# Kernel tuning notes

Measured on AMD Instinct MI355X. Metric: run time of the kernel, lower is better.

Reference implementation:

```python
import jax, jax.numpy as jnp
import numpy as np

EPS = 1e-8
NEG = -float(2 ** 31)

B, N, D = 8, 2048, 256  # batch, nodes, input_dim == output_dim


def setup_inputs() -> dict:
    key = jax.random.key(0)
    ks = jax.random.split(key, 8)
    x = jax.random.normal(ks[0], (B, N, D), dtype=jnp.float32)
    x_topic = jax.random.normal(ks[1], (B, N, D), dtype=jnp.float32)
    adj_mask = jax.random.randint(ks[2], (B, N, N), 0, 2, dtype=jnp.int32)
    s = 1.0 / np.sqrt(D)
    W = jax.random.uniform(ks[3], (D, D), minval=-s, maxval=s, dtype=jnp.float32)
    # GRUCell params (torch layout: [3*H, in] with gate order r, z, n)
    W_ih = jax.random.uniform(ks[4], (3 * D, D), minval=-s, maxval=s, dtype=jnp.float32)
    W_hh = jax.random.uniform(ks[5], (3 * D, D), minval=-s, maxval=s, dtype=jnp.float32)
    b_ih = jax.random.uniform(ks[6], (3 * D,), minval=-s, maxval=s, dtype=jnp.float32)
    b_hh = jax.random.uniform(ks[7], (3 * D,), minval=-s, maxval=s, dtype=jnp.float32)
    return {"adj_mask": adj_mask, "x": x, "x_topic": x_topic,
            "W": W, "W_ih": W_ih, "W_hh": W_hh, "b_ih": b_ih, "b_hh": b_hh}


def _gru_cell(inp, h, W_ih, W_hh, b_ih, b_hh):
    # torch.nn.GRUCell math, gate order (r, z, n)
    gi = inp @ W_ih.T + b_ih
    gh = h @ W_hh.T + b_hh
    i_r, i_z, i_n = jnp.split(gi, 3, axis=-1)
    h_r, h_z, h_n = jnp.split(gh, 3, axis=-1)
    r = jax.nn.sigmoid(i_r + h_r)
    z = jax.nn.sigmoid(i_z + h_z)
    n = jnp.tanh(i_n + r * h_n)
    return (1.0 - z) * n + z * h


def reference(adj_mask, x, x_topic, W, W_ih, W_hh, b_ih, b_hh):
    # Wh: [B, N, H]
    Wh = jnp.einsum('bnd,dh->bnh', x, W)
    # pairwise cosine similarity via normalized gram matrix (no N x N x D intermediate)
    nrm = jnp.linalg.norm(x_topic, axis=-1)            # [B, N]
    dots = jnp.einsum('bnd,bmd->bnm', x_topic, x_topic)
    e = dots / jnp.maximum(nrm[:, :, None] * nrm[:, None, :], EPS)
    scores = jnp.where(adj_mask > 0, e, NEG)
    attention = jax.nn.softmax(scores, axis=-1)        # [B, N, N]
    graph_out = jnp.einsum('bnm,bmh->bnh', attention, Wh)
    out = _gru_cell(graph_out, x, W_ih, W_hh, b_ih, b_hh)
    return out
```

## Files before the change

kernel.cpp:

```cpp
#include <hip/hip_runtime.h>
#include <hip/hip_bf16.h>

#define B_ 8
#define N_ 2048
#define D_ 256

using bf16 = __hip_bfloat16;
typedef short v8s __attribute__((ext_vector_type(8)));
typedef float v4f __attribute__((ext_vector_type(4)));
typedef float v16f __attribute__((ext_vector_type(16)));
typedef unsigned int u32;

__device__ __forceinline__ v4f mfma16(v8s a, v8s b, v4f c) {
  return __builtin_amdgcn_mfma_f32_16x16x32_bf16(a, b, c, 0, 0, 0);
}
__device__ __forceinline__ v16f mfma32(v8s a, v8s b, v16f c) {
  return __builtin_amdgcn_mfma_f32_32x32x16_bf16(a, b, c, 0, 0, 0);
}
__device__ __forceinline__ v8s ldb8(const bf16* p) {
  return *reinterpret_cast<const v8s*>(p);
}
__device__ __forceinline__ void glds16(const void* g, void* l) {
  __builtin_amdgcn_global_load_lds((const __attribute__((address_space(1))) u32*)g,
                                   (__attribute__((address_space(3))) u32*)l, 16, 0, 0);
}
__device__ __forceinline__ unsigned short f2bu(float f) {
  bf16 b = __float2bfloat16(f);
  return *reinterpret_cast<unsigned short*>(&b);
}
__device__ __forceinline__ float bs2f(short s) {
  union { u32 i; float f; } v; v.i = ((u32)(unsigned short)s) << 16; return v.f;
}
__device__ __forceinline__ float lo16(u32 u) { union {u32 i; float f;} v; v.i = u << 16; return v.f; }
__device__ __forceinline__ float hi16(u32 u) { union {u32 i; float f;} v; v.i = u & 0xffff0000u; return v.f; }
__device__ __forceinline__ u32 pack2(float a, float b) {
  return (u32)f2bu(a) | ((u32)f2bu(b) << 16);
}
__device__ __forceinline__ float fsigmoid(float x) { return 1.0f / (1.0f + __expf(-x)); }
__device__ __forceinline__ float ftanh(float x) {
  float ax = fabsf(x);
  float t = __expf(-2.0f * ax);
  float r = (1.0f - t) / (1.0f + t);
  return copysignf(r, x);
}

__global__ __launch_bounds__(256) void k_cvt(const float* __restrict__ src,
                                             bf16* __restrict__ dst, int n4) {
  int i = blockIdx.x * 256 + threadIdx.x;
  if (i >= n4) return;
  float4 v = reinterpret_cast<const float4*>(src)[i];
  ushort4 o;
  o.x = f2bu(v.x); o.y = f2bu(v.y); o.z = f2bu(v.z); o.w = f2bu(v.w);
  reinterpret_cast<ushort4*>(dst)[i] = o;
}

__global__ __launch_bounds__(256) void k_cvtn(const float* __restrict__ xt,
                                              bf16* __restrict__ dst) {
  int i = blockIdx.x * 256 + threadIdx.x;
  float4 v = reinterpret_cast<const float4*>(xt)[i];
  float s = v.x * v.x + v.y * v.y + v.z * v.z + v.w * v.w;
#pragma unroll
  for (int off = 32; off > 0; off >>= 1) s += __shfl_xor(s, off);
  float rinv = 1.0f / fmaxf(sqrtf(s), 1e-8f);
  ushort4 o;
  o.x = f2bu(v.x * rinv); o.y = f2bu(v.y * rinv);
  o.z = f2bu(v.z * rinv); o.w = f2bu(v.w * rinv);
  reinterpret_cast<ushort4*>(dst)[i] = o;
}

__global__ __launch_bounds__(256) void k_prep(const float* __restrict__ W,
                                              bf16* __restrict__ Wt,
                                              const float* __restrict__ Wih,
                                              bf16* __restrict__ Wih16,
                                              const float* __restrict__ Whh,
                                              bf16* __restrict__ Whh16) {
  int blk = blockIdx.x;
  if (blk < 256) {
    int idx = blk * 256 + threadIdx.x;
    int d = idx >> 8, h = idx & 255;
    Wt[h * 256 + d] = __float2bfloat16(W[idx]);
  } else if (blk < 448) {
    int i = (blk - 256) * 256 + threadIdx.x;
    float4 v = reinterpret_cast<const float4*>(Wih)[i];
    ushort4 o;
    o.x = f2bu(v.x); o.y = f2bu(v.y); o.z = f2bu(v.z); o.w = f2bu(v.w);
    reinterpret_cast<ushort4*>(Wih16)[i] = o;
  } else {
    int i = (blk - 448) * 256 + threadIdx.x;
    float4 v = reinterpret_cast<const float4*>(Whh)[i];
    ushort4 o;
    o.x = f2bu(v.x); o.y = f2bu(v.y); o.z = f2bu(v.z); o.w = f2bu(v.w);
    reinterpret_cast<ushort4*>(Whh16)[i] = o;
  }
}

__global__ __launch_bounds__(256) void k_packT(const int* __restrict__ adj,
                                               u32* __restrict__ maskT) {
  int bi = blockIdx.x;
  int bg = bi >> 1, half = bi & 1;
  const int* base = adj + (size_t)bg * 32 * 2048;
  int c0 = half * 1024 + threadIdx.x * 4;
  u32 w0 = 0, w1 = 0, w2 = 0, w3 = 0;
#pragma unroll 4
  for (int r = 0; r < 32; r++) {
    int4 v = *reinterpret_cast<const int4*>(base + r * 2048 + c0);
    w0 |= (u32)(v.x > 0) << r;
    w1 |= (u32)(v.y > 0) << r;
    w2 |= (u32)(v.z > 0) << r;
    w3 |= (u32)(v.w > 0) << r;
  }
  uint4 o; o.x = w0; o.y = w1; o.z = w2; o.w = w3;
  *reinterpret_cast<uint4*>(maskT + (size_t)bg * 2048 + c0) = o;
}

__global__ __launch_bounds__(256) void k_wht(const bf16* __restrict__ x,
                                             const bf16* __restrict__ Wt,
                                             bf16* __restrict__ WhT) {
  int wid = blockIdx.x * 4 + (threadIdx.x >> 6);
  int lane = threadIdx.x & 63, lr = lane & 15, quad = lane >> 4;
  int b = wid >> 9;
  int rem = wid & 511;
  int h0 = (rem >> 5) << 4;
  int m0 = (rem & 31) << 6;

  v8s a[8];
  const bf16* arow = Wt + (size_t)(h0 + lr) * D_ + quad * 8;
#pragma unroll
  for (int ks = 0; ks < 8; ks++) a[ks] = ldb8(arow + ks * 32);

  const bf16* xb = x + (size_t)b * N_ * D_;
#pragma unroll
  for (int mt = 0; mt < 4; mt++) {
    v4f acc = {0.f, 0.f, 0.f, 0.f};
    const bf16* brow = xb + (size_t)(m0 + mt * 16 + lr) * D_ + quad * 8;
#pragma unroll
    for (int ks = 0; ks < 8; ks++) acc = mfma16(a[ks], ldb8(brow + ks * 32), acc);
    bf16* o = WhT + ((size_t)b * D_ + h0 + quad * 4) * N_ + m0 + mt * 16 + lr;
#pragma unroll
    for (int r = 0; r < 4; r++) o[(size_t)r * N_] = __float2bfloat16(acc[r]);
  }
}

__global__ __launch_bounds__(256, 2) void k_attn(const bf16* __restrict__ xtn,
                                                 const u32* __restrict__ maskT,
                                                 const bf16* __restrict__ WhT,
                                                 bf16* __restrict__ po,
                                                 float* __restrict__ pls) {
  __shared__ __align__(16) bf16 xts[2][32 * 256];
  __shared__ __align__(16) bf16 whs[2][256 * 32];
  __shared__ __align__(16) bf16 pbuf[4][32 * 40];

  const int tid = threadIdx.x;
  const int w = tid >> 6, lane = tid & 63;
  const int l5 = lane >> 5, l31 = lane & 31;
  const int b = blockIdx.x & 7;
  const int nt = (blockIdx.x >> 3) & 15;
  const int mh = blockIdx.x >> 7;
  const int n0w = nt * 128 + w * 32;
  const int mbase = mh * 512;

  const bf16* xtb = xtn + (size_t)b * N_ * D_;
  const bf16* whb = WhT + (size_t)b * D_ * N_;

  v8s q[16];
  {
    const bf16* qrow = xtb + (size_t)(n0w + l31) * D_ + l5 * 8;
#pragma unroll
    for (int kt = 0; kt < 16; kt++) q[kt] = ldb8(qrow + kt * 16);
  }
  const u32* mrow = maskT + ((size_t)(b * 64 + nt * 4 + w)) * 2048 + mbase + l31;

  auto stage = [&](int d, int m0) {
    const char* gx = (const char*)(xtb + (size_t)m0 * D_);
    char* lx = ((char*)xts[d]) + w * 4096;
#pragma unroll
    for (int j = 0; j < 4; j++) {
      int m = w * 8 + j * 2 + l5;
      int gg = l31 ^ (m & 7);
      glds16(gx + (size_t)m * 512 + gg * 16, lx + j * 1024);
    }
    char* lw = ((char*)whs[d]) + w * 4096;
#pragma unroll
    for (int j = 0; j < 4; j++) {
      int h = w * 64 + j * 16 + (lane >> 2);
      int g = (lane & 3) ^ ((lane >> 3) & 3);
      glds16((const char*)(whb + (size_t)h * N_ + m0) + g * 16, lw + j * 1024);
    }
  };

  v16f o[8];
#pragma unroll
  for (int t = 0; t < 8; t++) o[t] = (v16f)(0.f);
  float lsum = 0.f;

  u32 mword = mrow[0];
  stage(0, mbase);

#pragma unroll 1
  for (int ii = 0; ii < 16; ii++) {
    const int d = ii & 1;
    __syncthreads();
    if (ii + 1 < 16) stage(1 - d, mbase + (ii + 1) * 32);
    u32 mnext = (ii + 1 < 16) ? mrow[(ii + 1) * 32] : 0u;

    v16f s = (v16f)(0.f);
    const bf16* xb = xts[d] + l31 * 256;
#pragma unroll
    for (int kt = 0; kt < 16; kt++) {
      int g = ((kt * 2 + l5) ^ (l31 & 7)) * 8;
      s = mfma32(q[kt], ldb8(xb + g), s);
    }

    bf16* pb = pbuf[w];
#pragma unroll
    for (int j = 0; j < 16; j++) {
      int row = (j & 3) + 8 * (j >> 2) + 4 * l5;
      float p = ((mword >> row) & 1u) ? __expf(s[j]) : 0.f;
      pb[row * 40 + l31] = __float2bfloat16(p);
    }
    mword = mnext;

    v8s pa0 = ldb8(pb + l31 * 40 + l5 * 8);
    v8s pa1 = ldb8(pb + l31 * 40 + 16 + l5 * 8);
#pragma unroll
    for (int e = 0; e < 8; e++) lsum += bs2f(pa0[e]) + bs2f(pa1[e]);

#pragma unroll
    for (int ht = 0; ht < 8; ht++) {
      const bf16* wb = whs[d] + (ht * 32 + l31) * 32;
      int s0 = (l5 ^ ((l31 >> 1) & 3)) * 8;
      int s1 = ((2 + l5) ^ ((l31 >> 1) & 3)) * 8;
      o[ht] = mfma32(pa0, ldb8(wb + s0), o[ht]);
      o[ht] = mfma32(pa1, ldb8(wb + s1), o[ht]);
    }
  }

  lsum += __shfl_xor(lsum, 32);
  if (lane < 32) pls[(size_t)mh * (B_ * N_) + b * N_ + n0w + l31] = lsum;

  bf16* pob = po + (size_t)mh * ((size_t)B_ * N_ * D_) + ((size_t)b * N_ + n0w) * D_;
#pragma unroll
  for (int ht = 0; ht < 8; ht++) {
#pragma unroll
    for (int j = 0; j < 16; j++) {
      int row = (j & 3) + 8 * (j >> 2) + 4 * l5;
      pob[(size_t)row * D_ + ht * 32 + l31] = __float2bfloat16(o[ht][j]);
    }
  }
}

__global__ __launch_bounds__(256) void k_comb(const bf16* __restrict__ po,
                                              const float* __restrict__ pls,
                                              bf16* __restrict__ gout) {
  int idx = blockIdx.x * 256 + threadIdx.x;
  int row = idx >> 5;
  const int R = B_ * N_;
  float inv = 1.0f / (pls[row] + pls[R + row] + pls[2 * R + row] + pls[3 * R + row]);
  const size_t S = (size_t)B_ * N_ * D_ / 8;
  const uint4* p = (const uint4*)po;
  uint4 a = p[idx], c = p[idx + S], e = p[idx + 2 * S], f = p[idx + 3 * S];
  uint4 o;
  o.x = pack2((lo16(a.x)+lo16(c.x)+lo16(e.x)+lo16(f.x)) * inv,
              (hi16(a.x)+hi16(c.x)+hi16(e.x)+hi16(f.x)) * inv);
  o.y = pack2((lo16(a.y)+lo16(c.y)+lo16(e.y)+lo16(f.y)) * inv,
              (hi16(a.y)+hi16(c.y)+hi16(e.y)+hi16(f.y)) * inv);
  o.z = pack2((lo16(a.z)+lo16(c.z)+lo16(e.z)+lo16(f.z)) * inv,
              (hi16(a.z)+hi16(c.z)+hi16(e.z)+hi16(f.z)) * inv);
  o.w = pack2((lo16(a.w)+lo16(c.w)+lo16(e.w)+lo16(f.w)) * inv,
              (hi16(a.w)+hi16(c.w)+hi16(e.w)+hi16(f.w)) * inv);
  reinterpret_cast<uint4*>(gout)[idx] = o;
}

__global__ __launch_bounds__(256) void k_gru(const bf16* __restrict__ gout,
                                             const bf16* __restrict__ x16,
                                             const bf16* __restrict__ Wih,
                                             const bf16* __restrict__ Whh,
                                             const float* __restrict__ bih,
                                             const float* __restrict__ bhh,
                                             const float* __restrict__ x32,
                                             float* __restrict__ out) {
  int wid = blockIdx.x * 4 + (threadIdx.x >> 6);
  int lane = threadIdx.x & 63, lr = lane & 15, quad = lane >> 4;
  int rs = wid >> 4;
  int col0 = (wid & 15) << 4;
  int row0 = rs << 6;
  int col = col0 + lr;

  float bi[3], bh[3];
#pragma unroll
  for (int g = 0; g < 3; g++) {
    bi[g] = bih[g * 256 + col];
    bh[g] = bhh[g * 256 + col];
  }
  v4f aI[3][4], aH[3][4];
#pragma unroll
  for (int g = 0; g < 3; g++)
#pragma unroll
    for (int rt = 0; rt < 4; rt++) {
      aI[g][rt] = (v4f){0, 0, 0, 0};
      aH[g][rt] = (v4f){0, 0, 0, 0};
    }

#pragma unroll 2
  for (int ks = 0; ks < 8; ks++) {
    int k0 = ks * 32 + quad * 8;
    v8s wI[3], wH[3];
#pragma unroll
    for (int g = 0; g < 3; g++) {
      wI[g] = ldb8(Wih + (size_t)(g * 256 + col0 + lr) * 256 + k0);
      wH[g] = ldb8(Whh + (size_t)(g * 256 + col0 + lr) * 256 + k0);
    }
#pragma unroll
    for (int rt = 0; rt < 4; rt++) {
      v8s aG = ldb8(gout + (size_t)(row0 + rt * 16 + lr) * 256 + k0);
      v8s aX = ldb8(x16 + (size_t)(row0 + rt * 16 + lr) * 256 + k0);
#pragma unroll
      for (int g = 0; g < 3; g++) {
        aI[g][rt] = mfma16(aG, wI[g], aI[g][rt]);
        aH[g][rt] = mfma16(aX, wH[g], aH[g][rt]);
      }
    }
  }

#pragma unroll
  for (int rt = 0; rt < 4; rt++) {
    int rowb = row0 + rt * 16 + quad * 4;
#pragma unroll
    for (int r = 0; r < 4; r++) {
      float ir  = aI[0][rt][r] + bi[0];
      float iz  = aI[1][rt][r] + bi[1];
      float in_ = aI[2][rt][r] + bi[2];
      float hr  = aH[0][rt][r] + bh[0];
      float hz  = aH[1][rt][r] + bh[1];
      float hn  = aH[2][rt][r] + bh[2];
      float rg = fsigmoid(ir + hr);
      float zg = fsigmoid(iz + hz);
      float ng = ftanh(in_ + rg * hn);
      float hv = x32[(size_t)(rowb + r) * 256 + col];
      out[(size_t)(rowb + r) * 256 + col] = (1.0f - zg) * ng + zg * hv;
    }
  }
}

extern "C" void kernel_launch(void* const* d_in, const int* in_sizes, int n_in,
                              void* d_out, int out_size, void* d_ws, size_t ws_size,
                              hipStream_t stream) {
  const int*   adj = (const int*)d_in[0];
  const float* x   = (const float*)d_in[1];
  const float* xt  = (const float*)d_in[2];
  const float* W   = (const float*)d_in[3];
  const float* Wih = (const float*)d_in[4];
  const float* Whh = (const float*)d_in[5];
  const float* bih = (const float*)d_in[6];
  const float* bhh = (const float*)d_in[7];
  float* out = (float*)d_out;

  char* ws = (char*)d_ws;
  bf16*  xb16   = (bf16*)(ws);
  bf16*  xtn    = (bf16*)(ws + (8u << 20));
  bf16*  gob    = (bf16*)(ws + (16u << 20));
  bf16*  WhT    = (bf16*)(ws + (24u << 20));
  bf16*  Wt     = (bf16*)(ws + (32u << 20));
  bf16*  Wih16  = (bf16*)(ws + (32u << 20) + (128u << 10));
  bf16*  Whh16  = (bf16*)(ws + (32u << 20) + (512u << 10));
  u32*   maskT  = (u32*)  (ws + (32u << 20) + (960u << 10));
  bf16*  po     = (bf16*) (ws + (40u << 20));
  float* pls    = (float*)(ws + (72u << 20));

  const int nBND4 = B_ * N_ * D_ / 4;
  k_packT<<<1024, 256, 0, stream>>>(adj, maskT);
  k_cvt<<<nBND4 / 256, 256, 0, stream>>>(x, xb16, nBND4);
  k_cvtn<<<nBND4 / 256, 256, 0, stream>>>(xt, xtn);
  k_prep<<<640, 256, 0, stream>>>(W, Wt, Wih, Wih16, Whh, Whh16);
  k_wht<<<1024, 256, 0, stream>>>(xb16, Wt, WhT);
  k_attn<<<512, 256, 0, stream>>>(xtn, maskT, WhT, po, pls);
  k_comb<<<2048, 256, 0, stream>>>(po, pls, gob);
  k_gru<<<1024, 256, 0, stream>>>(gob, xb16, Wih16, Whh16, bih, bhh, x, out);
}
```

Measured before the change: 396.3 us.

## Split attention key range 8 ways, single-buffer LDS, fuse cast kernels

```diff
diff --git a/kernel.cpp b/kernel.cpp
--- a/kernel.cpp
+++ b/kernel.cpp
@@ -44,28 +44,29 @@
   return copysignf(r, x);
 }
 
-__global__ __launch_bounds__(256) void k_cvt(const float* __restrict__ src,
-                                             bf16* __restrict__ dst, int n4) {
-  int i = blockIdx.x * 256 + threadIdx.x;
-  if (i >= n4) return;
-  float4 v = reinterpret_cast<const float4*>(src)[i];
-  ushort4 o;
-  o.x = f2bu(v.x); o.y = f2bu(v.y); o.z = f2bu(v.z); o.w = f2bu(v.w);
-  reinterpret_cast<ushort4*>(dst)[i] = o;
-}
-
-__global__ __launch_bounds__(256) void k_cvtn(const float* __restrict__ xt,
-                                              bf16* __restrict__ dst) {
-  int i = blockIdx.x * 256 + threadIdx.x;
-  float4 v = reinterpret_cast<const float4*>(xt)[i];
-  float s = v.x * v.x + v.y * v.y + v.z * v.z + v.w * v.w;
-#pragma unroll
-  for (int off = 32; off > 0; off >>= 1) s += __shfl_xor(s, off);
-  float rinv = 1.0f / fmaxf(sqrtf(s), 1e-8f);
-  ushort4 o;
-  o.x = f2bu(v.x * rinv); o.y = f2bu(v.y * rinv);
-  o.z = f2bu(v.z * rinv); o.w = f2bu(v.w * rinv);
-  reinterpret_cast<ushort4*>(dst)[i] = o;
+__global__ __launch_bounds__(256) void k_cast(const float* __restrict__ x,
+                                              bf16* __restrict__ xb16,
+                                              const float* __restrict__ xt,
+                                              bf16* __restrict__ xtn) {
+  int blk = blockIdx.x;
+  if (blk < 4096) {
+    int i = blk * 256 + threadIdx.x;
+    float4 v = reinterpret_cast<const float4*>(x)[i];
+    ushort4 o;
+    o.x = f2bu(v.x); o.y = f2bu(v.y); o.z = f2bu(v.z); o.w = f2bu(v.w);
+    reinterpret_cast<ushort4*>(xb16)[i] = o;
+  } else {
+    int i = (blk - 4096) * 256 + threadIdx.x;
+    float4 v = reinterpret_cast<const float4*>(xt)[i];
+    float s = v.x * v.x + v.y * v.y + v.z * v.z + v.w * v.w;
+#pragma unroll
+    for (int off = 32; off > 0; off >>= 1) s += __shfl_xor(s, off);
+    float rinv = 1.0f / fmaxf(sqrtf(s), 1e-8f);
+    ushort4 o;
+    o.x = f2bu(v.x * rinv); o.y = f2bu(v.y * rinv);
+    o.z = f2bu(v.z * rinv); o.w = f2bu(v.w * rinv);
+    reinterpret_cast<ushort4*>(xtn)[i] = o;
+  }
 }
 
 __global__ __launch_bounds__(256) void k_prep(const float* __restrict__ W,
@@ -141,13 +142,13 @@
   }
 }
 
-__global__ __launch_bounds__(256, 2) void k_attn(const bf16* __restrict__ xtn,
+__global__ __launch_bounds__(256, 3) void k_attn(const bf16* __restrict__ xtn,
                                                  const u32* __restrict__ maskT,
                                                  const bf16* __restrict__ WhT,
                                                  bf16* __restrict__ po,
                                                  float* __restrict__ pls) {
-  __shared__ __align__(16) bf16 xts[2][32 * 256];
-  __shared__ __align__(16) bf16 whs[2][256 * 32];
+  __shared__ __align__(16) bf16 xts[32 * 256];
+  __shared__ __align__(16) bf16 whs[256 * 32];
   __shared__ __align__(16) bf16 pbuf[4][32 * 40];
 
   const int tid = threadIdx.x;
@@ -157,7 +158,7 @@
   const int nt = (blockIdx.x >> 3) & 15;
   const int mh = blockIdx.x >> 7;
   const int n0w = nt * 128 + w * 32;
-  const int mbase = mh * 512;
+  const int mbase = mh * 256;
 
   const bf16* xtb = xtn + (size_t)b * N_ * D_;
   const bf16* whb = WhT + (size_t)b * D_ * N_;
@@ -170,16 +171,16 @@
   }
   const u32* mrow = maskT + ((size_t)(b * 64 + nt * 4 + w)) * 2048 + mbase + l31;
 
-  auto stage = [&](int d, int m0) {
+  auto stage = [&](int m0) {
     const char* gx = (const char*)(xtb + (size_t)m0 * D_);
-    char* lx = ((char*)xts[d]) + w * 4096;
+    char* lx = ((char*)xts) + w * 4096;
 #pragma unroll
     for (int j = 0; j < 4; j++) {
       int m = w * 8 + j * 2 + l5;
       int gg = l31 ^ (m & 7);
       glds16(gx + (size_t)m * 512 + gg * 16, lx + j * 1024);
     }
-    char* lw = ((char*)whs[d]) + w * 4096;
+    char* lw = ((char*)whs) + w * 4096;
 #pragma unroll
     for (int j = 0; j < 4; j++) {
       int h = w * 64 + j * 16 + (lane >> 2);
@@ -194,17 +195,16 @@
   float lsum = 0.f;
 
   u32 mword = mrow[0];
-  stage(0, mbase);
 
 #pragma unroll 1
-  for (int ii = 0; ii < 16; ii++) {
-    const int d = ii & 1;
+  for (int ii = 0; ii < 8; ii++) {
     __syncthreads();
-    if (ii + 1 < 16) stage(1 - d, mbase + (ii + 1) * 32);
-    u32 mnext = (ii + 1 < 16) ? mrow[(ii + 1) * 32] : 0u;
+    stage(mbase + ii * 32);
+    u32 mnext = (ii + 1 < 8) ? mrow[(ii + 1) * 32] : 0u;
+    __syncthreads();
 
     v16f s = (v16f)(0.f);
-    const bf16* xb = xts[d] + l31 * 256;
+    const bf16* xb = xts + l31 * 256;
 #pragma unroll
     for (int kt = 0; kt < 16; kt++) {
       int g = ((kt * 2 + l5) ^ (l31 & 7)) * 8;
@@ -227,7 +227,7 @@
 
 #pragma unroll
     for (int ht = 0; ht < 8; ht++) {
-      const bf16* wb = whs[d] + (ht * 32 + l31) * 32;
+      const bf16* wb = whs + (ht * 32 + l31) * 32;
       int s0 = (l5 ^ ((l31 >> 1) & 3)) * 8;
       int s1 = ((2 + l5) ^ ((l31 >> 1) & 3)) * 8;
       o[ht] = mfma32(pa0, ldb8(wb + s0), o[ht]);
@@ -255,19 +255,26 @@
   int idx = blockIdx.x * 256 + threadIdx.x;
   int row = idx >> 5;
   const int R = B_ * N_;
-  float inv = 1.0f / (pls[row] + pls[R + row] + pls[2 * R + row] + pls[3 * R + row]);
+  float d = 0.f;
+#pragma unroll
+  for (int s = 0; s < 8; s++) d += pls[s * R + row];
+  float inv = 1.0f / d;
   const size_t S = (size_t)B_ * N_ * D_ / 8;
   const uint4* p = (const uint4*)po;
-  uint4 a = p[idx], c = p[idx + S], e = p[idx + 2 * S], f = p[idx + 3 * S];
+  float ax = 0, bx = 0, ay = 0, by = 0, az = 0, bz = 0, aw = 0, bw = 0;
+#pragma unroll
+  for (int s = 0; s < 8; s++) {
+    uint4 v = p[idx + s * S];
+    ax += lo16(v.x); bx += hi16(v.x);
+    ay += lo16(v.y); by += hi16(v.y);
+    az += lo16(v.z); bz += hi16(v.z);
+    aw += lo16(v.w); bw += hi16(v.w);
+  }
   uint4 o;
-  o.x = pack2((lo16(a.x)+lo16(c.x)+lo16(e.x)+lo16(f.x)) * inv,
-              (hi16(a.x)+hi16(c.x)+hi16(e.x)+hi16(f.x)) * inv);
-  o.y = pack2((lo16(a.y)+lo16(c.y)+lo16(e.y)+lo16(f.y)) * inv,
-              (hi16(a.y)+hi16(c.y)+hi16(e.y)+hi16(f.y)) * inv);
-  o.z = pack2((lo16(a.z)+lo16(c.z)+lo16(e.z)+lo16(f.z)) * inv,
-              (hi16(a.z)+hi16(c.z)+hi16(e.z)+hi16(f.z)) * inv);
-  o.w = pack2((lo16(a.w)+lo16(c.w)+lo16(e.w)+lo16(f.w)) * inv,
-              (hi16(a.w)+hi16(c.w)+hi16(e.w)+hi16(f.w)) * inv);
+  o.x = pack2(ax * inv, bx * inv);
+  o.y = pack2(ay * inv, by * inv);
+  o.z = pack2(az * inv, bz * inv);
+  o.w = pack2(aw * inv, bw * inv);
   reinterpret_cast<uint4*>(gout)[idx] = o;
 }
 
@@ -301,7 +308,7 @@
       aH[g][rt] = (v4f){0, 0, 0, 0};
     }
 
-#pragma unroll 2
+#pragma unroll 4
   for (int ks = 0; ks < 8; ks++) {
     int k0 = ks * 32 + quad * 8;
     v8s wI[3], wH[3];
@@ -363,17 +370,15 @@
   bf16*  Wt     = (bf16*)(ws + (32u << 20));
   bf16*  Wih16  = (bf16*)(ws + (32u << 20) + (128u << 10));
   bf16*  Whh16  = (bf16*)(ws + (32u << 20) + (512u << 10));
-  u32*   maskT  = (u32*)  (ws + (32u << 20) + (960u << 10));
+  float* pls    = (float*)(ws + (32u << 20) + (896u << 10));
+  u32*   maskT  = (u32*)  (ws + (36u << 20));
   bf16*  po     = (bf16*) (ws + (40u << 20));
-  float* pls    = (float*)(ws + (72u << 20));
-
-  const int nBND4 = B_ * N_ * D_ / 4;
+
   k_packT<<<1024, 256, 0, stream>>>(adj, maskT);
-  k_cvt<<<nBND4 / 256, 256, 0, stream>>>(x, xb16, nBND4);
-  k_cvtn<<<nBND4 / 256, 256, 0, stream>>>(xt, xtn);
+  k_cast<<<8192, 256, 0, stream>>>(x, xb16, xt, xtn);
   k_prep<<<640, 256, 0, stream>>>(W, Wt, Wih, Wih16, Whh, Whh16);
   k_wht<<<1024, 256, 0, stream>>>(xb16, Wt, WhT);
-  k_attn<<<512, 256, 0, stream>>>(xtn, maskT, WhT, po, pls);
+  k_attn<<<1024, 256, 0, stream>>>(xtn, maskT, WhT, po, pls);
   k_comb<<<2048, 256, 0, stream>>>(po, pls, gob);
   k_gru<<<1024, 256, 0, stream>>>(gob, xb16, Wih16, Whh16, bih, bhh, x, out);
 }
```

Result: slower. 555.6 us (+40.2%).
